# Performance work log

Hardware: AMD Instinct MI355X
Metric: run time of the kernel (lower is better)

Reference implementation:

```python
import jax, jax.numpy as jnp
import numpy as np

B, L, D_IN, D_MODEL, D_STATE, D_DISCR, KER = 2, 1024, 512, 1024, 16, 64, 4


def setup_inputs() -> dict:
    ks = jax.random.split(jax.random.key(0), 9)
    s = 0.02
    return {
        "seq": jax.random.normal(ks[0], (B, L, D_IN), jnp.float32),
        "W_in": jax.random.normal(ks[1], (2 * D_MODEL, D_IN), jnp.float32) * s,
        "W_out": jax.random.normal(ks[2], (D_IN, D_MODEL), jnp.float32) * s,
        "W_B": jax.random.normal(ks[3], (D_STATE, D_MODEL), jnp.float32) * s,
        "W_C": jax.random.normal(ks[4], (D_STATE, D_MODEL), jnp.float32) * s,
        "W_D1": jax.random.normal(ks[5], (D_DISCR, D_MODEL), jnp.float32) * s,
        "W_D2": jax.random.normal(ks[6], (D_MODEL, D_DISCR), jnp.float32) * s,
        "conv_w": jax.random.normal(ks[7], (D_MODEL, 1, KER), jnp.float32) * 0.1,
        "conv_b": jax.random.normal(ks[8], (D_MODEL,), jnp.float32) * 0.01,
        "A": jnp.tile(jnp.arange(1, D_STATE + 1, dtype=jnp.float32), (D_MODEL, 1)),
        "D": jnp.ones((D_MODEL,), jnp.float32),
    }


def _causal_depthwise_conv(x, w, b):
    # x: [B, L, D] -> torch Conv1d(groups=D, padding=KER-1) truncated to first L outputs
    x = jnp.swapaxes(x, 1, 2)  # [B, D, L]
    y = jax.lax.conv_general_dilated(
        x, w, window_strides=(1,), padding=[(KER - 1, 0)],
        dimension_numbers=("NCH", "OIH", "NCH"), feature_group_count=D_MODEL)
    y = y + b[None, :, None]
    return jnp.swapaxes(y, 1, 2)  # [B, L, D]


def _ssm(x, W_B, W_C, W_D1, W_D2, A, D):
    # x: [B, L, D]
    exp_negA = jnp.exp(-A)                                  # [D, S]
    Bm = jnp.einsum("bld,sd->bls", x, W_B)                  # [B, L, S]
    Cm = jnp.einsum("bld,sd->bls", x, W_C)                  # [B, L, S]
    delta = jax.nn.softplus(D + jnp.einsum("ble,de->bld", jnp.einsum("bld,ed->ble", x, W_D1), W_D2))  # [B, L, D]
    A_bar = exp_negA[None, None] * delta[..., None]         # [B, L, D, S]
    X = Bm[:, :, None, :] * delta[..., None] * x[..., None]  # [B, L, D, S]

    def comb(c1, c2):
        a1, x1 = c1
        a2, x2 = c2
        return a1 * a2, a2 * x1 + x2

    _, h = jax.lax.associative_scan(comb, (A_bar, X), axis=1)  # h: [B, L, D, S]
    y = jnp.einsum("blds,bls->bld", h, Cm)
    return y + D * x


def reference(seq, W_in, W_out, W_B, W_C, W_D1, W_D2, conv_w, conv_b, A, D):
    ab = jnp.einsum("bli,oi->blo", seq, W_in)   # [B, L, 2*D_MODEL]
    a, b = ab[..., :D_MODEL], ab[..., D_MODEL:]
    a = jax.nn.silu(_causal_depthwise_conv(a, conv_w, conv_b))
    a = _ssm(a, W_B, W_C, W_D1, W_D2, A, D)
    out = a * jax.nn.silu(b)
    return jnp.einsum("bld,od->blo", out, W_out)  # [B, L, D_IN]
```

## Files before the change

kernel.cpp:

```cpp
#include <hip/hip_runtime.h>
#include <hip/hip_bf16.h>

typedef short short8 __attribute__((ext_vector_type(8)));
typedef short short4v __attribute__((ext_vector_type(4)));
typedef float float4v __attribute__((ext_vector_type(4)));

#define B_   2
#define L_   1024
#define DIN  512
#define DM   1024
#define DS   16
#define DD   64
#define KER_ 4
#define NROW (B_*L_)

#define SD   4
#define SC   128
#define SLC  8
#define NSEG 8

__device__ __forceinline__ float silu_f(float v){ return v / (1.f + expf(-v)); }

__device__ __forceinline__ short2 f2bf2(float a, float b) {
  __hip_bfloat162 h = __float22bfloat162_rn(float2{a, b});
  union { __hip_bfloat162 h; short2 s; } u; u.h = h; return u.s;
}
__device__ __forceinline__ short f2bf1(float a) {
  __hip_bfloat16 h = __float2bfloat16(a);
  union { __hip_bfloat16 h; short s; } u; u.h = h; return u.s;
}
__device__ __forceinline__ short8 pack8(const float4& x0, const float4& x1) {
  short2 s0 = f2bf2(x0.x, x0.y), s1 = f2bf2(x0.z, x0.w);
  short2 s2 = f2bf2(x1.x, x1.y), s3 = f2bf2(x1.z, x1.w);
  return short8{ s0.x, s0.y, s1.x, s1.y, s2.x, s2.y, s3.x, s3.y };
}
__device__ __forceinline__ float bf2f(short s) {
  union { unsigned u; float f; } v; v.u = ((unsigned)(unsigned short)s) << 16; return v.f;
}

__global__ __launch_bounds__(512)
void gemm1_k(const float* __restrict__ seq, const float* __restrict__ Win,
             __hip_bfloat16* __restrict__ ab, float* __restrict__ pall) {
  __shared__ short As[128 * 40];
  __shared__ short Bs[128 * 40];
  const int tid  = threadIdx.x;
  {
    int zi = (blockIdx.y * 16 + blockIdx.x) * 1024 + tid * 2;
    if (zi < NROW * 96) { pall[zi] = 0.f; pall[zi + 1] = 0.f; }
  }
  const int lane = tid & 63;
  const int wave = tid >> 6;
  const int r16  = lane & 15;
  const int quad = lane >> 4;
  const int m0 = blockIdx.y * 128;
  const int n0 = blockIdx.x * 128;
  const int wm = wave & 1;
  const int wn = wave >> 1;
  float4v acc[4][2];
#pragma unroll
  for (int i = 0; i < 4; i++)
#pragma unroll
    for (int j = 0; j < 2; j++) acc[i][j] = (float4v){0.f, 0.f, 0.f, 0.f};
  const int row = tid >> 2, q = tid & 3;
  float4 pfA0, pfA1, pfB0, pfB1;
  auto ldu = [&](int k0) {
    const float4* pa = (const float4*)(seq + (size_t)(m0 + row) * DIN + k0 + q * 8);
    pfA0 = pa[0]; pfA1 = pa[1];
    const float4* pb = (const float4*)(Win + (size_t)(n0 + row) * DIN + k0 + q * 8);
    pfB0 = pb[0]; pfB1 = pb[1];
  };
  auto stu = [&]() {
    *(short8*)&As[row * 40 + q * 8] = pack8(pfA0, pfA1);
    *(short8*)&Bs[row * 40 + q * 8] = pack8(pfB0, pfB1);
  };
  ldu(0);
  for (int k0 = 0; k0 < DIN; k0 += 32) {
    stu();
    __syncthreads();
    if (k0 + 32 < DIN) ldu(k0 + 32);
    short8 afr[4], bfr[2];
#pragma unroll
    for (int mi = 0; mi < 4; mi++)
      afr[mi] = *(const short8*)&As[(wm * 64 + mi * 16 + r16) * 40 + quad * 8];
#pragma unroll
    for (int ni = 0; ni < 2; ni++)
      bfr[ni] = *(const short8*)&Bs[(wn * 32 + ni * 16 + r16) * 40 + quad * 8];
#pragma unroll
    for (int mi = 0; mi < 4; mi++)
#pragma unroll
      for (int ni = 0; ni < 2; ni++)
        acc[mi][ni] = __builtin_amdgcn_mfma_f32_16x16x32_bf16(afr[mi], bfr[ni], acc[mi][ni], 0, 0, 0);
    __syncthreads();
  }
#pragma unroll
  for (int mi = 0; mi < 4; mi++)
#pragma unroll
    for (int ni = 0; ni < 2; ni++) {
      int gn = n0 + wn * 32 + ni * 16 + r16;
#pragma unroll
      for (int r = 0; r < 4; r++) {
        int gm = m0 + wm * 64 + mi * 16 + quad * 4 + r;
        ab[(size_t)gm * (2 * DM) + gn] = __float2bfloat16(acc[mi][ni][r]);
      }
    }
}

__global__ __launch_bounds__(256)
void convproj_k(const __hip_bfloat16* __restrict__ ab, const float* __restrict__ cw,
                const float* __restrict__ cb, const float* __restrict__ WB,
                const float* __restrict__ WC, const float* __restrict__ WD1,
                float* __restrict__ xt, short* __restrict__ gt,
                float* __restrict__ pall) {
  __shared__ char smraw[12800];
  const int blk = blockIdx.x;
  const int tid = threadIdx.x;

  if (blk < 1024) {
    short* tile = (short*)smraw;
    const int n0 = (blk & 31) * 64;
    const int d0 = (blk >> 5) * 64;
    const int l0 = n0 & (L_ - 1);
    for (int u = tid; u < 67 * 8; u += 256) {
      int r = u >> 3, c8 = u & 7;
      int l = l0 - 3 + r;
      short8 v = short8{0, 0, 0, 0, 0, 0, 0, 0};
      if (l >= 0 && r < 67)
        v = *(const short8*)(ab + (size_t)(n0 - l0 + l) * (2 * DM) + d0 + c8 * 8);
      *(short8*)&tile[r * 72 + c8 * 8] = v;
    }
    __syncthreads();
    const int i  = tid & 63;
    const int dl = tid >> 6;
    if (d0 < DM) {
#pragma unroll
      for (int p8 = 0; p8 < 2; p8++) {
        const int dc0 = dl * 16 + p8 * 8;
        short8 t0 = *(const short8*)&tile[(i + 0) * 72 + dc0];
        short8 t1 = *(const short8*)&tile[(i + 1) * 72 + dc0];
        short8 t2 = *(const short8*)&tile[(i + 2) * 72 + dc0];
        short8 t3 = *(const short8*)&tile[(i + 3) * 72 + dc0];
#pragma unroll
        for (int e = 0; e < 8; e++) {
          int d = d0 + dc0 + e;
          float4 w = *(const float4*)(cw + d * 4);
          float a = cb[d];
          a += bf2f(t0[e]) * w.x;
          a += bf2f(t1[e]) * w.y;
          a += bf2f(t2[e]) * w.z;
          a += bf2f(t3[e]) * w.w;
          xt[(size_t)d * NROW + n0 + i] = silu_f(a);
        }
      }
    } else {
#pragma unroll
      for (int p8 = 0; p8 < 2; p8++) {
        const int dc0 = dl * 16 + p8 * 8;
        short8 v = *(const short8*)&tile[(i + 3) * 72 + dc0];
#pragma unroll
        for (int e = 0; e < 8; e++)
          gt[(size_t)(d0 - DM + dc0 + e) * NROW + n0 + i] = v[e];
      }
    }
    return;
  }

  short* As = (short*)smraw;
  short* Bs = As + 64 * 40;
  const int b2   = blk - 1024;
  const int lane = tid & 63;
  const int wave = tid >> 6;
  const int r16  = lane & 15;
  const int quad = lane >> 4;
  const int m0   = (b2 & 31) * 64;
  const int kbeg = (b2 >> 5) * 128;
  float4v acc[6];
#pragma unroll
  for (int i = 0; i < 6; i++) acc[i] = (float4v){0.f, 0.f, 0.f, 0.f};

  short8 ta[KER_];
  float4 pf0[2], pf1[2];
  const int arow = tid >> 2, aq = tid & 3;
  const int an = m0 + arow, al = an & (L_ - 1), abq = an >> 10;

  auto ldu_a = [&](int k0) {
#pragma unroll
    for (int t = 0; t < KER_; t++) {
      int ll = al - (KER_ - 1) + t;
      if (ll >= 0)
        ta[t] = *(const short8*)(ab + (size_t)(abq * L_ + ll) * (2 * DM) + k0 + aq * 8);
      else
        ta[t] = short8{0, 0, 0, 0, 0, 0, 0, 0};
    }
  };
  auto stu_a = [&](int k0) {
    float r8[8];
#pragma unroll
    for (int e = 0; e < 8; e++) {
      int d = k0 + aq * 8 + e;
      float4 w = *(const float4*)(cw + d * 4);
      float a = cb[d];
      a += bf2f(ta[0][e]) * w.x;
      a += bf2f(ta[1][e]) * w.y;
      a += bf2f(ta[2][e]) * w.z;
      a += bf2f(ta[3][e]) * w.w;
      r8[e] = silu_f(a);
    }
    *(short8*)&As[arow * 40 + aq * 8] =
        pack8(float4{r8[0], r8[1], r8[2], r8[3]}, float4{r8[4], r8[5], r8[6], r8[7]});
  };
  auto ldu_b = [&](int j, int k0) {
    int u = tid + j * 256;
    if (u >= 640) return;
    int v = u - 256, row = v >> 2, q = v & 3;
    const float* bp = (row < 16) ? (WB + (size_t)row * DM)
                    : (row < 32) ? (WC + (size_t)(row - 16) * DM)
                                 : (WD1 + (size_t)(row - 32) * DM);
    const float4* p = (const float4*)(bp + k0 + q * 8);
    pf0[j - 1] = p[0]; pf1[j - 1] = p[1];
  };
  auto stu_b = [&](int j) {
    int u = tid + j * 256;
    if (u >= 640) return;
    int v = u - 256, row = v >> 2, q = v & 3;
    *(short8*)&Bs[row * 40 + q * 8] = pack8(pf0[j - 1], pf1[j - 1]);
  };

  ldu_a(kbeg); ldu_b(1, kbeg); ldu_b(2, kbeg);
  for (int k0 = kbeg; k0 < kbeg + 128; k0 += 32) {
    stu_a(k0); stu_b(1); stu_b(2);
    __syncthreads();
    if (k0 + 32 < kbeg + 128) { ldu_a(k0 + 32); ldu_b(1, k0 + 32); ldu_b(2, k0 + 32); }
    short8 afr = *(const short8*)&As[(wave * 16 + r16) * 40 + quad * 8];
#pragma unroll
    for (int ni = 0; ni < 6; ni++) {
      short8 bfr = *(const short8*)&Bs[(ni * 16 + r16) * 40 + quad * 8];
      acc[ni] = __builtin_amdgcn_mfma_f32_16x16x32_bf16(afr, bfr, acc[ni], 0, 0, 0);
    }
    __syncthreads();
  }
#pragma unroll
  for (int ni = 0; ni < 6; ni++) {
    int gn = ni * 16 + r16;
#pragma unroll
    for (int r = 0; r < 4; r++) {
      int gm = m0 + wave * 16 + quad * 4 + r;
      atomicAdd(&pall[(size_t)gm * 96 + gn], acc[ni][r]);
    }
  }
}

__global__ __launch_bounds__(256)
void delta_k(const float* __restrict__ t1, const float* __restrict__ WD2,
             const float* __restrict__ Dv, float* __restrict__ dltT) {
  __shared__ short As[64 * 40];
  __shared__ short Bs[64 * 40];
  const int tid  = threadIdx.x;
  const int lane = tid & 63;
  const int wave = tid >> 6;
  const int r16  = lane & 15;
  const int quad = lane >> 4;
  const int m0 = blockIdx.y * 64;
  const int n0 = blockIdx.x * 64;
  const int wm = wave & 1, wn = wave >> 1;
  float4v acc[2][2];
#pragma unroll
  for (int i = 0; i < 2; i++)
#pragma unroll
    for (int j = 0; j < 2; j++) acc[i][j] = (float4v){0.f, 0.f, 0.f, 0.f};
  float4 pf0[2], pf1[2];
  auto ldu = [&](int j, int k0) {
    int u = tid + j * 256;
    const float4* p;
    if (u < 256) { int row = u >> 2, q = u & 3;
      p = (const float4*)(t1 + (size_t)(m0 + row) * 96 + k0 + q * 8);
    } else { int v = u - 256; int row = v >> 2, q = v & 3;
      p = (const float4*)(WD2 + (size_t)(n0 + row) * DD + k0 + q * 8);
    }
    pf0[j] = p[0]; pf1[j] = p[1];
  };
  auto stu = [&](int j) {
    int u = tid + j * 256;
    short8 s = pack8(pf0[j], pf1[j]);
    if (u < 256) { int row = u >> 2, q = u & 3; *(short8*)&As[row * 40 + q * 8] = s; }
    else { int v = u - 256; int row = v >> 2, q = v & 3; *(short8*)&Bs[row * 40 + q * 8] = s; }
  };
  ldu(0, 0); ldu(1, 0);
  for (int k0 = 0; k0 < DD; k0 += 32) {
    stu(0); stu(1);
    __syncthreads();
    if (k0 + 32 < DD) { ldu(0, k0 + 32); ldu(1, k0 + 32); }
    short8 afr[2], bfr[2];
#pragma unroll
    for (int mi = 0; mi < 2; mi++)
      afr[mi] = *(const short8*)&As[(wm * 32 + mi * 16 + r16) * 40 + quad * 8];
#pragma unroll
    for (int ni = 0; ni < 2; ni++)
      bfr[ni] = *(const short8*)&Bs[(wn * 32 + ni * 16 + r16) * 40 + quad * 8];
#pragma unroll
    for (int mi = 0; mi < 2; mi++)
#pragma unroll
      for (int ni = 0; ni < 2; ni++)
        acc[mi][ni] = __builtin_amdgcn_mfma_f32_16x16x32_bf16(afr[mi], bfr[ni], acc[mi][ni], 0, 0, 0);
    __syncthreads();
  }
#pragma unroll
  for (int mi = 0; mi < 2; mi++)
#pragma unroll
    for (int ni = 0; ni < 2; ni++) {
      int gn = n0 + wn * 32 + ni * 16 + r16;
      float dvn = Dv[gn];
#pragma unroll
      for (int r = 0; r < 4; r++) {
        int gm = m0 + wm * 32 + mi * 16 + quad * 4 + r;
        float v = acc[mi][ni][r] + dvn;
        v = fmaxf(v, 0.f) + log1pf(expf(-fabsf(v)));
        dltT[(size_t)gn * NROW + gm] = v;
      }
    }
}

__global__ __launch_bounds__(512, 2)
void scan_fused_k(const float* __restrict__ xt, const float* __restrict__ dltT,
                  const float* __restrict__ pall, const float* __restrict__ A,
                  const float* __restrict__ Dv, const short* __restrict__ gt,
                  short* __restrict__ soutb) {
  __shared__ float Pl[DS * SD][SC + 1];
  __shared__ float Hl[DS * SD][SC + 1];
  __shared__ float Ps[DS * SD][NSEG + 1];
  __shared__ float Hs[DS * SD][NSEG + 1];
  const int blk = blockIdx.x;
  const int b   = blk >> 8;
  const int d0  = (blk & 255) * SD;
  const int dd  = threadIdx.x & (SD - 1);
  const int c   = threadIdx.x >> 2;
  const int d   = d0 + dd;

  float e[DS];
#pragma unroll
  for (int s = 0; s < DS; s++) e[s] = expf(-A[d * DS + s]);

  const int nbase = b * L_ + c * SLC;
  const float* xrow = xt   + (size_t)d * NROW;
  const float* drow = dltT + (size_t)d * NROW;
  const short* grow = gt   + (size_t)d * NROW;

  float h[DS];
#pragma unroll
  for (int s = 0; s < DS; s++) h[s] = 0.f;
  float pdl = 1.f;
#pragma unroll
  for (int q = 0; q < SLC / 4; q++) {
    const int n = nbase + q * 4;
    float4 x4 = *(const float4*)(xrow + n);
    float4 d4 = *(const float4*)(drow + n);
    float4 bq[4][4];
#pragma unroll
    for (int t = 0; t < 4; t++) {
      const float4* pp = (const float4*)(pall + (size_t)(n + t) * 96);
      bq[t][0] = pp[0]; bq[t][1] = pp[1]; bq[t][2] = pp[2]; bq[t][3] = pp[3];
    }
#pragma unroll
    for (int t = 0; t < 4; t++) {
      float dl = (&d4.x)[t], xv = (&x4.x)[t];
      float dx = dl * xv;
      pdl *= dl;
      float bmv[DS] = { bq[t][0].x, bq[t][0].y, bq[t][0].z, bq[t][0].w,
                        bq[t][1].x, bq[t][1].y, bq[t][1].z, bq[t][1].w,
                        bq[t][2].x, bq[t][2].y, bq[t][2].z, bq[t][2].w,
                        bq[t][3].x, bq[t][3].y, bq[t][3].z, bq[t][3].w };
#pragma unroll
      for (int s = 0; s < DS; s++)
        h[s] = (e[s] * dl) * h[s] + bmv[s] * dx;
    }
  }
#pragma unroll
  for (int s = 0; s < DS; s++) {
    float e2 = e[s] * e[s], e4 = e2 * e2, e8 = e4 * e4;
    Pl[dd * DS + s][c] = e8 * pdl;
    Hl[dd * DS + s][c] = h[s];
  }
  __syncthreads();

  {
    const int seg = threadIdx.x >> 6;
    const int cmb = threadIdx.x & 63;
    float* Prow = &Pl[cmb][0];
    float* Hrow = &Hl[cmb][0];
    float Pa = 1.f, Ha = 0.f;
#pragma unroll
    for (int i = 0; i < SC / NSEG; i++) {
      int c2 = seg * (SC / NSEG) + i;
      float p = Prow[c2], hh = Hrow[c2];
      Prow[c2] = Pa;
      Hrow[c2] = Ha;
      Ha = p * Ha + hh;
      Pa *= p;
    }
    Ps[cmb][seg] = Pa;
    Hs[cmb][seg] = Ha;
  }
  __syncthreads();

  if (threadIdx.x < DS * SD) {
    float* Pr = &Ps[threadIdx.x][0];
    float* Hr = &Hs[threadIdx.x][0];
    float H = 0.f;
#pragma unroll
    for (int g = 0; g < NSEG; g++) {
      float p = Pr[g], hh = Hr[g];
      Hr[g] = H;
      H = p * H + hh;
    }
  }
  __syncthreads();

  {
    const int g = c >> 4;
#pragma unroll
    for (int s = 0; s < DS; s++)
      h[s] = Pl[dd * DS + s][c] * Hs[dd * DS + s][g] + Hl[dd * DS + s][c];
  }
  const float Dd = Dv[d];
#pragma unroll
  for (int q = 0; q < SLC / 4; q++) {
    const int n = nbase + q * 4;
    float4 x4 = *(const float4*)(xrow + n);
    float4 d4 = *(const float4*)(drow + n);
    short4v g4 = *(const short4v*)(grow + n);
    float4 bq[4][4], cq[4][4];
#pragma unroll
    for (int t = 0; t < 4; t++) {
      const float4* pp = (const float4*)(pall + (size_t)(n + t) * 96);
      bq[t][0] = pp[0]; bq[t][1] = pp[1]; bq[t][2] = pp[2]; bq[t][3] = pp[3];
      cq[t][0] = pp[4]; cq[t][1] = pp[5]; cq[t][2] = pp[6]; cq[t][3] = pp[7];
    }
#pragma unroll
    for (int t = 0; t < 4; t++) {
      float dl = (&d4.x)[t], xv = (&x4.x)[t];
      float dx = dl * xv;
      float bmv[DS] = { bq[t][0].x, bq[t][0].y, bq[t][0].z, bq[t][0].w,
                        bq[t][1].x, bq[t][1].y, bq[t][1].z, bq[t][1].w,
                        bq[t][2].x, bq[t][2].y, bq[t][2].z, bq[t][2].w,
                        bq[t][3].x, bq[t][3].y, bq[t][3].z, bq[t][3].w };
      float cmv[DS] = { cq[t][0].x, cq[t][0].y, cq[t][0].z, cq[t][0].w,
                        cq[t][1].x, cq[t][1].y, cq[t][1].z, cq[t][1].w,
                        cq[t][2].x, cq[t][2].y, cq[t][2].z, cq[t][2].w,
                        cq[t][3].x, cq[t][3].y, cq[t][3].z, cq[t][3].w };
      float y = 0.f;
#pragma unroll
      for (int s = 0; s < DS; s++) {
        h[s] = (e[s] * dl) * h[s] + bmv[s] * dx;
        y += h[s] * cmv[s];
      }
      y += Dd * xv;
      float gg = bf2f(g4[t]);
      soutb[(size_t)(n + t) * DM + d] = f2bf1(y * silu_f(gg));
    }
  }
}

__global__ __launch_bounds__(256)
void gemm2_k(const short* __restrict__ soutb, const float* __restrict__ Wout,
             float* __restrict__ out) {
  __shared__ short As[64 * 40];
  __shared__ short Bs[32 * 40];
  const int tid  = threadIdx.x;
  const int lane = tid & 63;
  const int wave = tid >> 6;
  const int r16  = lane & 15;
  const int quad = lane >> 4;
  const int m0 = blockIdx.y * 64;
  const int n0 = blockIdx.x * 32;
  const int wm = wave & 1, wn = wave >> 1;
  float4v acc[2];
  acc[0] = (float4v){0.f, 0.f, 0.f, 0.f};
  acc[1] = (float4v){0.f, 0.f, 0.f, 0.f};
  short8 pa;
  float4 pf0, pf1;
  auto ldu = [&](int k0) {
    {
      int row = tid >> 2, q = tid & 3;
      pa = *(const short8*)(soutb + (size_t)(m0 + row) * DM + k0 + q * 8);
    }
    if (tid < 128) {
      int row = tid >> 2, q = tid & 3;
      const float4* p = (const float4*)(Wout + (size_t)(n0 + row) * DM + k0 + q * 8);
      pf0 = p[0]; pf1 = p[1];
    }
  };
  auto stu = [&]() {
    { int row = tid >> 2, q = tid & 3; *(short8*)&As[row * 40 + q * 8] = pa; }
    if (tid < 128) { int row = tid >> 2, q = tid & 3; *(short8*)&Bs[row * 40 + q * 8] = pack8(pf0, pf1); }
  };
  ldu(0);
  for (int k0 = 0; k0 < DM; k0 += 32) {
    stu();
    __syncthreads();
    if (k0 + 32 < DM) ldu(k0 + 32);
    short8 afr[2], bfr;
    afr[0] = *(const short8*)&As[(wm * 32 + r16) * 40 + quad * 8];
    afr[1] = *(const short8*)&As[(wm * 32 + 16 + r16) * 40 + quad * 8];
    bfr    = *(const short8*)&Bs[(wn * 16 + r16) * 40 + quad * 8];
    acc[0] = __builtin_amdgcn_mfma_f32_16x16x32_bf16(afr[0], bfr, acc[0], 0, 0, 0);
    acc[1] = __builtin_amdgcn_mfma_f32_16x16x32_bf16(afr[1], bfr, acc[1], 0, 0, 0);
    __syncthreads();
  }
#pragma unroll
  for (int mi = 0; mi < 2; mi++)
#pragma unroll
    for (int r = 0; r < 4; r++)
      out[(size_t)(m0 + wm * 32 + mi * 16 + quad * 4 + r) * DIN + n0 + wn * 16 + r16] = acc[mi][r];
}

extern "C" void kernel_launch(void* const* d_in, const int* in_sizes, int n_in,
                              void* d_out, int out_size, void* d_ws, size_t ws_size,
                              hipStream_t stream) {
  const float* seq  = (const float*)d_in[0];
  const float* Win  = (const float*)d_in[1];
  const float* Wout = (const float*)d_in[2];
  const float* WB   = (const float*)d_in[3];
  const float* WC   = (const float*)d_in[4];
  const float* WD1  = (const float*)d_in[5];
  const float* WD2  = (const float*)d_in[6];
  const float* cw   = (const float*)d_in[7];
  const float* cb   = (const float*)d_in[8];
  const float* A    = (const float*)d_in[9];
  const float* Dv   = (const float*)d_in[10];
  float* out = (float*)d_out;

  float* ws = (float*)d_ws;
  __hip_bfloat16* ab = (__hip_bfloat16*)ws;
  float* xt   = ws   + 2097152;
  short* gt   = (short*)(xt + 2097152);
  float* dltT = (float*)(gt + 2097152);
  float* pall = dltT + 2097152;
  short* soutb = (short*)(pall + 196608);
  float* t1   = pall + 32;

  gemm1_k<<<dim3(16, 16), 512, 0, stream>>>(seq, Win, ab, pall);
  convproj_k<<<1280, 256, 0, stream>>>(ab, cw, cb, WB, WC, WD1, xt, gt, pall);
  delta_k<<<dim3(16, 32), 256, 0, stream>>>(t1, WD2, Dv, dltT);
  scan_fused_k<<<B_ * (DM / SD), 512, 0, stream>>>(xt, dltT, pall, A, Dv, gt, soutb);
  gemm2_k<<<dim3(16, 32), 256, 0, stream>>>(soutb, Wout, out);
}
```

Before: 161.1 us.

## Use wave-shuffle scan across chunks and widen gemm2 output tile

The scan kernel remaps threads so each wave handles one channel across 64 consecutive chunks, and replaces the three-phase shared-memory chunk scan with a wavefront shuffle-up prefix scan plus a single cross-wave carry through a tiny shared array. This removes the large LDS staging arrays and two block barriers, and drops the occupancy hint from launch bounds. gemm2 now computes 64x64 tiles with four MFMAs per wave per k-step, which halves the block count and improves operand reuse. The cost is many more shuffle instructions, higher register pressure in the scan, and fewer, larger gemm2 blocks.

```diff
diff --git a/kernel.cpp b/kernel.cpp
--- a/kernel.cpp
+++ b/kernel.cpp
@@ -17,7 +17,6 @@
 #define SD   4
 #define SC   128
 #define SLC  8
-#define NSEG 8
 
 __device__ __forceinline__ float silu_f(float v){ return v / (1.f + expf(-v)); }
 
@@ -319,21 +318,22 @@
     }
 }
 
-__global__ __launch_bounds__(512, 2)
+__global__ __launch_bounds__(512)
 void scan_fused_k(const float* __restrict__ xt, const float* __restrict__ dltT,
                   const float* __restrict__ pall, const float* __restrict__ A,
                   const float* __restrict__ Dv, const short* __restrict__ gt,
                   short* __restrict__ soutb) {
-  __shared__ float Pl[DS * SD][SC + 1];
-  __shared__ float Hl[DS * SD][SC + 1];
-  __shared__ float Ps[DS * SD][NSEG + 1];
-  __shared__ float Hs[DS * SD][NSEG + 1];
-  const int blk = blockIdx.x;
-  const int b   = blk >> 8;
-  const int d0  = (blk & 255) * SD;
-  const int dd  = threadIdx.x & (SD - 1);
-  const int c   = threadIdx.x >> 2;
-  const int d   = d0 + dd;
+  __shared__ float Tot[SD][DS][2];
+  const int blk  = blockIdx.x;
+  const int b    = blk >> 8;
+  const int d0   = (blk & 255) * SD;
+  const int tid  = threadIdx.x;
+  const int lane = tid & 63;
+  const int wave = tid >> 6;
+  const int dd   = wave & 3;
+  const int hf   = wave >> 2;
+  const int c    = hf * 64 + lane;
+  const int d    = d0 + dd;
 
   float e[DS];
 #pragma unroll
@@ -353,73 +353,62 @@
     const int n = nbase + q * 4;
     float4 x4 = *(const float4*)(xrow + n);
     float4 d4 = *(const float4*)(drow + n);
-    float4 bq[4][4];
 #pragma unroll
     for (int t = 0; t < 4; t++) {
       const float4* pp = (const float4*)(pall + (size_t)(n + t) * 96);
-      bq[t][0] = pp[0]; bq[t][1] = pp[1]; bq[t][2] = pp[2]; bq[t][3] = pp[3];
-    }
-#pragma unroll
-    for (int t = 0; t < 4; t++) {
+      float4 b0 = pp[0], b1 = pp[1], b2 = pp[2], b3 = pp[3];
       float dl = (&d4.x)[t], xv = (&x4.x)[t];
       float dx = dl * xv;
       pdl *= dl;
-      float bmv[DS] = { bq[t][0].x, bq[t][0].y, bq[t][0].z, bq[t][0].w,
-                        bq[t][1].x, bq[t][1].y, bq[t][1].z, bq[t][1].w,
-                        bq[t][2].x, bq[t][2].y, bq[t][2].z, bq[t][2].w,
-                        bq[t][3].x, bq[t][3].y, bq[t][3].z, bq[t][3].w };
+      float bmv[DS] = { b0.x, b0.y, b0.z, b0.w, b1.x, b1.y, b1.z, b1.w,
+                        b2.x, b2.y, b2.z, b2.w, b3.x, b3.y, b3.z, b3.w };
 #pragma unroll
       for (int s = 0; s < DS; s++)
         h[s] = (e[s] * dl) * h[s] + bmv[s] * dx;
     }
   }
+
+  float P[DS], H[DS];
 #pragma unroll
   for (int s = 0; s < DS; s++) {
-    float e2 = e[s] * e[s], e4 = e2 * e2, e8 = e4 * e4;
-    Pl[dd * DS + s][c] = e8 * pdl;
-    Hl[dd * DS + s][c] = h[s];
+    float e2 = e[s] * e[s], e4 = e2 * e2;
+    P[s] = (e4 * e4) * pdl;
+    H[s] = h[s];
+  }
+
+#pragma unroll
+  for (int off = 1; off < 64; off <<= 1) {
+#pragma unroll
+    for (int s = 0; s < DS; s++) {
+      float Pp = __shfl_up(P[s], off);
+      float Hp = __shfl_up(H[s], off);
+      if (lane >= off) { H[s] = fmaf(P[s], Hp, H[s]); P[s] *= Pp; }
+    }
+  }
+
+  float Pex[DS], Hex[DS];
+#pragma unroll
+  for (int s = 0; s < DS; s++) {
+    Pex[s] = __shfl_up(P[s], 1);
+    Hex[s] = __shfl_up(H[s], 1);
+  }
+  if (lane == 0) {
+#pragma unroll
+    for (int s = 0; s < DS; s++) { Pex[s] = 1.f; Hex[s] = 0.f; }
+  }
+  if (hf == 0 && lane == 63) {
+#pragma unroll
+    for (int s = 0; s < DS; s++) { Tot[dd][s][0] = P[s]; Tot[dd][s][1] = H[s]; }
   }
   __syncthreads();
-
-  {
-    const int seg = threadIdx.x >> 6;
-    const int cmb = threadIdx.x & 63;
-    float* Prow = &Pl[cmb][0];
-    float* Hrow = &Hl[cmb][0];
-    float Pa = 1.f, Ha = 0.f;
-#pragma unroll
-    for (int i = 0; i < SC / NSEG; i++) {
-      int c2 = seg * (SC / NSEG) + i;
-      float p = Prow[c2], hh = Hrow[c2];
-      Prow[c2] = Pa;
-      Hrow[c2] = Ha;
-      Ha = p * Ha + hh;
-      Pa *= p;
-    }
-    Ps[cmb][seg] = Pa;
-    Hs[cmb][seg] = Ha;
-  }
-  __syncthreads();
-
-  if (threadIdx.x < DS * SD) {
-    float* Pr = &Ps[threadIdx.x][0];
-    float* Hr = &Hs[threadIdx.x][0];
-    float H = 0.f;
-#pragma unroll
-    for (int g = 0; g < NSEG; g++) {
-      float p = Pr[g], hh = Hr[g];
-      Hr[g] = H;
-      H = p * H + hh;
-    }
-  }
-  __syncthreads();
-
-  {
-    const int g = c >> 4;
+  if (hf == 1) {
 #pragma unroll
     for (int s = 0; s < DS; s++)
-      h[s] = Pl[dd * DS + s][c] * Hs[dd * DS + s][g] + Hl[dd * DS + s][c];
-  }
+      Hex[s] = fmaf(Pex[s], Tot[dd][s][1], Hex[s]);
+  }
+
+#pragma unroll
+  for (int s = 0; s < DS; s++) h[s] = Hex[s];
   const float Dd = Dv[d];
 #pragma unroll
   for (int q = 0; q < SLC / 4; q++) {
@@ -427,25 +416,17 @@
     float4 x4 = *(const float4*)(xrow + n);
     float4 d4 = *(const float4*)(drow + n);
     short4v g4 = *(const short4v*)(grow + n);
-    float4 bq[4][4], cq[4][4];
 #pragma unroll
     for (int t = 0; t < 4; t++) {
       const float4* pp = (const float4*)(pall + (size_t)(n + t) * 96);
-      bq[t][0] = pp[0]; bq[t][1] = pp[1]; bq[t][2] = pp[2]; bq[t][3] = pp[3];
-      cq[t][0] = pp[4]; cq[t][1] = pp[5]; cq[t][2] = pp[6]; cq[t][3] = pp[7];
-    }
-#pragma unroll
-    for (int t = 0; t < 4; t++) {
+      float4 b0 = pp[0], b1 = pp[1], b2 = pp[2], b3 = pp[3];
+      float4 c0 = pp[4], c1 = pp[5], c2 = pp[6], c3 = pp[7];
       float dl = (&d4.x)[t], xv = (&x4.x)[t];
       float dx = dl * xv;
-      float bmv[DS] = { bq[t][0].x, bq[t][0].y, bq[t][0].z, bq[t][0].w,
-                        bq[t][1].x, bq[t][1].y, bq[t][1].z, bq[t][1].w,
-                        bq[t][2].x, bq[t][2].y, bq[t][2].z, bq[t][2].w,
-                        bq[t][3].x, bq[t][3].y, bq[t][3].z, bq[t][3].w };
-      float cmv[DS] = { cq[t][0].x, cq[t][0].y, cq[t][0].z, cq[t][0].w,
-                        cq[t][1].x, cq[t][1].y, cq[t][1].z, cq[t][1].w,
-                        cq[t][2].x, cq[t][2].y, cq[t][2].z, cq[t][2].w,
-                        cq[t][3].x, cq[t][3].y, cq[t][3].z, cq[t][3].w };
+      float bmv[DS] = { b0.x, b0.y, b0.z, b0.w, b1.x, b1.y, b1.z, b1.w,
+                        b2.x, b2.y, b2.z, b2.w, b3.x, b3.y, b3.z, b3.w };
+      float cmv[DS] = { c0.x, c0.y, c0.z, c0.w, c1.x, c1.y, c1.z, c1.w,
+                        c2.x, c2.y, c2.z, c2.w, c3.x, c3.y, c3.z, c3.w };
       float y = 0.f;
 #pragma unroll
       for (int s = 0; s < DS; s++) {
@@ -463,53 +444,62 @@
 void gemm2_k(const short* __restrict__ soutb, const float* __restrict__ Wout,
              float* __restrict__ out) {
   __shared__ short As[64 * 40];
-  __shared__ short Bs[32 * 40];
+  __shared__ short Bs[64 * 40];
   const int tid  = threadIdx.x;
   const int lane = tid & 63;
   const int wave = tid >> 6;
   const int r16  = lane & 15;
   const int quad = lane >> 4;
   const int m0 = blockIdx.y * 64;
-  const int n0 = blockIdx.x * 32;
+  const int n0 = blockIdx.x * 64;
   const int wm = wave & 1, wn = wave >> 1;
-  float4v acc[2];
-  acc[0] = (float4v){0.f, 0.f, 0.f, 0.f};
-  acc[1] = (float4v){0.f, 0.f, 0.f, 0.f};
+  float4v acc[2][2];
+#pragma unroll
+  for (int i = 0; i < 2; i++)
+#pragma unroll
+    for (int j = 0; j < 2; j++) acc[i][j] = (float4v){0.f, 0.f, 0.f, 0.f};
+  const int row = tid >> 2, q = tid & 3;
   short8 pa;
   float4 pf0, pf1;
   auto ldu = [&](int k0) {
-    {
-      int row = tid >> 2, q = tid & 3;
-      pa = *(const short8*)(soutb + (size_t)(m0 + row) * DM + k0 + q * 8);
-    }
-    if (tid < 128) {
-      int row = tid >> 2, q = tid & 3;
-      const float4* p = (const float4*)(Wout + (size_t)(n0 + row) * DM + k0 + q * 8);
-      pf0 = p[0]; pf1 = p[1];
-    }
+    pa = *(const short8*)(soutb + (size_t)(m0 + row) * DM + k0 + q * 8);
+    const float4* p = (const float4*)(Wout + (size_t)(n0 + row) * DM + k0 + q * 8);
+    pf0 = p[0]; pf1 = p[1];
   };
   auto stu = [&]() {
-    { int row = tid >> 2, q = tid & 3; *(short8*)&As[row * 40 + q * 8] = pa; }
-    if (tid < 128) { int row = tid >> 2, q = tid & 3; *(short8*)&Bs[row * 40 + q * 8] = pack8(pf0, pf1); }
+    *(short8*)&As[row * 40 + q * 8] = pa;
+    *(short8*)&Bs[row * 40 + q * 8] = pack8(pf0, pf1);
   };
   ldu(0);
   for (int k0 = 0; k0 < DM; k0 += 32) {
     stu();
     __syncthreads();
     if (k0 + 32 < DM) ldu(k0 + 32);
-    short8 afr[2], bfr;
-    afr[0] = *(const short8*)&As[(wm * 32 + r16) * 40 + quad * 8];
-    afr[1] = *(const short8*)&As[(wm * 32 + 16 + r16) * 40 + quad * 8];
-    bfr    = *(const short8*)&Bs[(wn * 16 + r16) * 40 + quad * 8];
-    acc[0] = __builtin_amdgcn_mfma_f32_16x16x32_bf16(afr[0], bfr, acc[0], 0, 0, 0);
-    acc[1] = __builtin_amdgcn_mfma_f32_16x16x32_bf16(afr[1], bfr, acc[1], 0, 0, 0);
+    short8 afr[2], bfr[2];
+#pragma unroll
+    for (int mi = 0; mi < 2; mi++)
+      afr[mi] = *(const short8*)&As[(wm * 32 + mi * 16 + r16) * 40 + quad * 8];
+#pragma unroll
+    for (int ni = 0; ni < 2; ni++)
+      bfr[ni] = *(const short8*)&Bs[(wn * 32 + ni * 16 + r16) * 40 + quad * 8];
+#pragma unroll
+    for (int mi = 0; mi < 2; mi++)
+#pragma unroll
+      for (int ni = 0; ni < 2; ni++)
+        acc[mi][ni] = __builtin_amdgcn_mfma_f32_16x16x32_bf16(afr[mi], bfr[ni], acc[mi][ni], 0, 0, 0);
     __syncthreads();
   }
 #pragma unroll
   for (int mi = 0; mi < 2; mi++)
 #pragma unroll
-    for (int r = 0; r < 4; r++)
-      out[(size_t)(m0 + wm * 32 + mi * 16 + quad * 4 + r) * DIN + n0 + wn * 16 + r16] = acc[mi][r];
+    for (int ni = 0; ni < 2; ni++) {
+      int gn = n0 + wn * 32 + ni * 16 + r16;
+#pragma unroll
+      for (int r = 0; r < 4; r++) {
+        int gm = m0 + wm * 32 + mi * 16 + quad * 4 + r;
+        out[(size_t)gm * DIN + gn] = acc[mi][ni][r];
+      }
+    }
 }
 
 extern "C" void kernel_launch(void* const* d_in, const int* in_sizes, int n_in,
@@ -541,5 +531,5 @@
   convproj_k<<<1280, 256, 0, stream>>>(ab, cw, cb, WB, WC, WD1, xt, gt, pall);
   delta_k<<<dim3(16, 32), 256, 0, stream>>>(t1, WD2, Dv, dltT);
   scan_fused_k<<<B_ * (DM / SD), 512, 0, stream>>>(xt, dltT, pall, A, Dv, gt, soutb);
-  gemm2_k<<<dim3(16, 32), 256, 0, stream>>>(soutb, Wout, out);
-}
+  gemm2_k<<<dim3(8, 32), 256, 0, stream>>>(soutb, Wout, out);
+}
```

Result: slower. 196.6 us (+22.1%).
